# Performance work log

Measured on AMD Instinct MI355X. Metric: run time of the kernel, lower is better.

## Reference

```python
import jax, jax.numpy as jnp
import numpy as np

B, N = 128, 1024            # batch, sample_count
MIN_S, MAX_S, STEP = 4.0, 104.0, 1.0  # scale range -> S = 101 scales
OUT_H, OUT_W = 200, 200     # output_size


def morlet_kernels():
    # scales = tf.range(min_scale, max_scale+1, step)
    scales = jnp.arange(MIN_S, MAX_S + 1.0, STEP, dtype=jnp.float32)  # (S,)
    t = jnp.arange(N, dtype=jnp.float32) - (N - 1.0) / 2.0            # centered time
    times = t[None, :] / scales[:, None]                               # (S, N)
    return jnp.exp(-0.5 * times ** 2) * jnp.cos(5.0 * times)          # morlet


def setup_inputs() -> dict:
    key = jax.random.key(0)
    x = jax.random.normal(key, (B, N), dtype=jnp.float32)
    kernels = morlet_kernels()  # (S, N), non-trainable param built in build()
    return {"x": x, "kernels": kernels}


def reference(x, kernels):
    # x: (B, N) signals; kernels: (S, N) scaled wavelets.
    # Original per-sample op: conv1d(kernels[S,N,1], filter=reverse(x)[N,1,1], SAME)
    # -> correlation of each wavelet row with the reversed signal (= convolution with x).
    n = x.shape[1]
    pad_l = (n - 1) // 2           # TF 'SAME' padding, stride 1, filter length n
    pad_r = (n - 1) - pad_l
    x_rev = x[:, ::-1]
    # One grouped conv: lhs=(S,1,N) NCW, rhs=(B,1,N) OIW -> out (S,B,N)
    res = jax.lax.conv_general_dilated(
        kernels[:, None, :], x_rev[:, None, :],
        window_strides=(1,), padding=[(pad_l, pad_r)],
        dimension_numbers=("NCW", "OIW", "NCW"))
    res = jnp.transpose(res, (1, 0, 2))  # (B, S, N)
    # global (per-sample) min-max normalization
    mn = jnp.min(res, axis=(1, 2), keepdims=True)
    mx = jnp.max(res, axis=(1, 2), keepdims=True)
    res_norm = (res - mn) / (mx - mn)
    img = res_norm[..., None]  # (B, S, N, 1)
    # tf.image.resize default: bilinear, antialias=False, half-pixel centers
    out = jax.image.resize(img, (img.shape[0], OUT_H, OUT_W, 1),
                           method="bilinear", antialias=False)
    return out
```

## Files before the change

kernel.cpp:

```cpp
#include <hip/hip_runtime.h>
#include <hip/hip_bf16.h>

#define NB 128
#define NS 101
#define NW 1024
#define OH 200
#define OW 200

typedef __bf16 bf16x8 __attribute__((ext_vector_type(8)));
typedef float f32x4 __attribute__((ext_vector_type(4)));

__device__ __forceinline__ void gload_lds16(const void* gsrc, void* ldst) {
    __builtin_amdgcn_global_load_lds(
        (const __attribute__((address_space(1))) void*)gsrc,
        (__attribute__((address_space(3))) void*)ldst, 16, 0, 0);
}

__device__ __forceinline__ unsigned encf(float f) {
    unsigned u = __float_as_uint(f);
    return (u & 0x80000000u) ? ~u : (u | 0x80000000u);
}
__device__ __forceinline__ float decf(unsigned e) {
    unsigned u = (e & 0x80000000u) ? (e ^ 0x80000000u) : ~e;
    return __uint_as_float(u);
}

__global__ __launch_bounds__(256) void prep_kernel(const float* __restrict__ K,
                                                   ushort* __restrict__ Kbf,
                                                   unsigned* __restrict__ mm) {
    int blk = blockIdx.x;
    if (blk < 112) {
        int c = threadIdx.x * 4;
        float4 v = make_float4(0.f, 0.f, 0.f, 0.f);
        if (blk < NS) v = *(const float4*)(K + (size_t)blk * NW + c);
        ushort4 o;
        __hip_bfloat16 h;
        h = __float2bfloat16(v.x); o.x = reinterpret_cast<const ushort&>(h);
        h = __float2bfloat16(v.y); o.y = reinterpret_cast<const ushort&>(h);
        h = __float2bfloat16(v.z); o.z = reinterpret_cast<const ushort&>(h);
        h = __float2bfloat16(v.w); o.w = reinterpret_cast<const ushort&>(h);
        *(ushort4*)(Kbf + (size_t)blk * NW + c) = o;
    } else {
        int t = threadIdx.x;
        mm[t] = (t < NB) ? 0xFFFFFFFFu : 0u;
    }
}


#define STAGE_T(t, lo, hi, base)                                              \
    _Pragma("unroll")                                                         \
    for (int s = (lo); s <= (hi); ++s) {                                      \
        if ((((base) + s - (lo)) & 7) == wv)                                  \
            gload_lds16(Kbf + (size_t)(16 * (t) + n) * NW + 32 * s + 8 * g,   \
                        &A_lds[((base) + s - (lo)) * 512]);                   \
    }

#define MFMA_T(t, lo, hi, base, ti)                                           \
    if (s >= (lo) && s <= (hi)) {                                             \
        bf16x8 af = *(const bf16x8*)&A_lds[((base) + s - (lo)) * 512 + lane * 8]; \
        _Pragma("unroll")                                                     \
        for (int nt = 0; nt < 8; ++nt)                                        \
            acc[ti][nt] = __builtin_amdgcn_mfma_f32_16x16x32_bf16(            \
                af, ring[(2 * s - nt) & 7], acc[ti][nt], 0, 0, 0);            \
    }

#define EPI_T(t, ti)                                                          \
    _Pragma("unroll")                                                         \
    for (int nt = 0; nt < 8; ++nt) {                                          \
        _Pragma("unroll")                                                     \
        for (int r = 0; r < 4; ++r) {                                         \
            const int row = 16 * (t) + 4 * g + r;                             \
            if (row < NS) {                                                   \
                float v = acc[ti][nt][r];                                     \
                mn = fminf(mn, v); mx = fmaxf(mx, v);                         \
                rb[(size_t)row * NW + wbase + 16 * nt + n] = __float2bfloat16(v); \
            }                                                                 \
        }                                                                     \
    }

__global__ __launch_bounds__(512, 2) void conv_mfma(
        const float* __restrict__ x, const ushort* __restrict__ Kbf,
        __hip_bfloat16* __restrict__ res, unsigned* __restrict__ mm) {
    __shared__ __align__(16) ushort A_lds[84 * 512];
    __shared__ __align__(16) ushort xSh[8 * 2056];

    const int tid = threadIdx.x;
    const int bid = blockIdx.x;
    const int cls = bid >> 7;
    const int b = bid & 127;
    const int wv = tid >> 6;
    const int lane = tid & 63;
    const int n = lane & 15;
    const int g = lane >> 4;

    {
        const float* xb = x + (size_t)b * NW;
        for (int idx = tid; idx < 8 * 257; idx += 512) {
            int dlt = idx / 257;
            int i0 = (idx % 257) * 8;
            union { ushort us[8]; uint4 v; } pk;
            #pragma unroll
            for (int j = 0; j < 8; ++j) {
                int ir = i0 + j + dlt;
                float f = (ir >= 512 && ir < 1536) ? xb[1535 - ir] : 0.0f;
                __hip_bfloat16 h = __float2bfloat16(f);
                pk.us[j] = reinterpret_cast<const ushort&>(h);
            }
            *reinterpret_cast<uint4*>(&xSh[dlt * 2056 + i0]) = pk.v;
        }
    }

    if (cls == 0) {
        STAGE_T(0, 12, 19, 0)
        STAGE_T(1,  9, 22, 8)
        STAGE_T(3,  3, 28, 22)
        STAGE_T(4,  0, 31, 48)
    } else {
        STAGE_T(2,  6, 25, 0)
        STAGE_T(5,  0, 31, 20)
        STAGE_T(6,  0, 31, 52)
    }
    __syncthreads();

    const int dlt = (7 - n) & 7;
    const int wbase = wv * 128;
    const ushort* bp = xSh + dlt * 2056 + (1023 - wbase - n + 8 * g - dlt);

    float mn = 3.4e38f, mx = -3.4e38f;
    __hip_bfloat16* rb = res + (size_t)b * NS * NW;

    if (cls == 0) {
        f32x4 acc[4][8];
        #pragma unroll
        for (int ti = 0; ti < 4; ++ti)
            #pragma unroll
            for (int nt = 0; nt < 8; ++nt)
                acc[ti][nt] = (f32x4){0.f, 0.f, 0.f, 0.f};
        bf16x8 ring[8];
        #pragma unroll
        for (int f = -7; f <= 0; ++f)
            ring[f & 7] = *(const bf16x8*)(bp + 16 * f);
        #pragma unroll
        for (int s = 0; s < 32; ++s) {
            if (s > 0) {
                ring[(2 * s - 1) & 7] = *(const bf16x8*)(bp + 16 * (2 * s - 1));
                ring[(2 * s) & 7]     = *(const bf16x8*)(bp + 16 * (2 * s));
            }
            MFMA_T(0, 12, 19, 0, 0)
            MFMA_T(1,  9, 22, 8, 1)
            MFMA_T(3,  3, 28, 22, 2)
            MFMA_T(4,  0, 31, 48, 3)
        }
        EPI_T(0, 0)
        EPI_T(1, 1)
        EPI_T(3, 2)
        EPI_T(4, 3)
    } else {
        f32x4 acc[3][8];
        #pragma unroll
        for (int ti = 0; ti < 3; ++ti)
            #pragma unroll
            for (int nt = 0; nt < 8; ++nt)
                acc[ti][nt] = (f32x4){0.f, 0.f, 0.f, 0.f};
        bf16x8 ring[8];
        #pragma unroll
        for (int f = -7; f <= 0; ++f)
            ring[f & 7] = *(const bf16x8*)(bp + 16 * f);
        #pragma unroll
        for (int s = 0; s < 32; ++s) {
            if (s > 0) {
                ring[(2 * s - 1) & 7] = *(const bf16x8*)(bp + 16 * (2 * s - 1));
                ring[(2 * s) & 7]     = *(const bf16x8*)(bp + 16 * (2 * s));
            }
            MFMA_T(2,  6, 25, 0, 0)
            MFMA_T(5,  0, 31, 20, 1)
            MFMA_T(6,  0, 31, 52, 2)
        }
        EPI_T(2, 0)
        EPI_T(5, 1)
        EPI_T(6, 2)
    }

    #pragma unroll
    for (int off = 32; off > 0; off >>= 1) {
        mn = fminf(mn, __shfl_down(mn, off));
        mx = fmaxf(mx, __shfl_down(mx, off));
    }
    if (lane == 0) {
        atomicMin(&mm[b], encf(mn));
        atomicMax(&mm[NB + b], encf(mx));
    }
}

__global__ __launch_bounds__(256) void resize_h(
        const __hip_bfloat16* __restrict__ res, float* __restrict__ tmp) {
    int idx = blockIdx.x * 256 + threadIdx.x;
    if (idx >= NB * NS * OW) return;
    const int j = idx % OW;
    const int s = (idx / OW) % NS;
    const int b = idx / (OW * NS);
    const float xx = (j + 0.5f) * (1024.0f / 200.0f) - 0.5f;
    const float xf = floorf(xx);
    const float fx = xx - xf;
    int j0 = (int)xf, j1 = j0 + 1;
    j0 = max(0, min(NW - 1, j0)); j1 = max(0, min(NW - 1, j1));
    const __hip_bfloat16* rp = res + ((size_t)b * NS + s) * NW;
    tmp[idx] = (1.f - fx) * __bfloat162float(rp[j0]) + fx * __bfloat162float(rp[j1]);
}

__global__ __launch_bounds__(256) void resize_v(
        const float* __restrict__ tmp, const unsigned* __restrict__ mm,
        float* __restrict__ out) {
    int idx = blockIdx.x * 256 + threadIdx.x;
    if (idx >= NB * OH * OW) return;
    const int j = idx % OW;
    const int i = (idx / OW) % OH;
    const int b = idx / (OW * OH);
    const float mn = decf(mm[b]);
    const float inv = 1.0f / (decf(mm[NB + b]) - mn);
    const float y = (i + 0.5f) * (101.0f / 200.0f) - 0.5f;
    const float yf = floorf(y);
    const float fy = y - yf;
    int i0 = (int)yf, i1 = i0 + 1;
    i0 = max(0, min(NS - 1, i0)); i1 = max(0, min(NS - 1, i1));
    const float* tp = tmp + (size_t)b * NS * OW;
    float v = (1.f - fy) * tp[i0 * OW + j] + fy * tp[i1 * OW + j];
    out[idx] = (v - mn) * inv;
}

extern "C" void kernel_launch(void* const* d_in, const int* in_sizes, int n_in,
                              void* d_out, int out_size, void* d_ws, size_t ws_size,
                              hipStream_t stream) {
    const float* x = (const float*)d_in[0];
    const float* K = (const float*)d_in[1];
    float* out = (float*)d_out;

    char* ws = (char*)d_ws;
    __hip_bfloat16* res = (__hip_bfloat16*)ws;
    size_t off = (size_t)NB * NS * NW * 2;
    unsigned* mm = (unsigned*)(ws + off);
    ushort* Kbf = (ushort*)(ws + off + 1024);
    float* tmp = (float*)(ws + off + 1024 + (size_t)112 * NW * 2);

    hipLaunchKernelGGL(prep_kernel, dim3(113), dim3(256), 0, stream, K, Kbf, mm);
    hipLaunchKernelGGL(conv_mfma, dim3(256), dim3(512), 0, stream, x, Kbf, res, mm);
    const int t1 = NB * NS * OW;
    hipLaunchKernelGGL(resize_h, dim3((t1 + 255) / 256), dim3(256), 0, stream, res, tmp);
    const int t2 = NB * OH * OW;
    hipLaunchKernelGGL(resize_v, dim3((t2 + 255) / 256), dim3(256), 0, stream, tmp, mm, out);
}
```

Measured before the change: 107.0 us.

## Fuse horizontal resize into conv epilogue via LDS staging

The conv kernel now stages each 16-row accumulator tile in shared memory as fp32 and performs the horizontal bilinear resize in place, writing the small 200-wide intermediate directly. This removes the full-resolution bf16 result buffer round trip and the separate resize_h launch. In exchange, LDS usage grows to about 116 KB and launch bounds drop to one block per CU, which lowers occupancy and adds barriers in the epilogue. As a side effect the resize reads fp32 values instead of bf16-rounded ones.

New measurement: 103.6 us. -3.2%, faster.

```diff
diff --git a/kernel.cpp b/kernel.cpp
--- a/kernel.cpp
+++ b/kernel.cpp
@@ -6,6 +6,7 @@
 #define NW 1024
 #define OH 200
 #define OW 200
+#define EPS 1034
 
 typedef __bf16 bf16x8 __attribute__((ext_vector_type(8)));
 typedef float f32x4 __attribute__((ext_vector_type(4)));
@@ -65,24 +66,42 @@
     }
 
 #define EPI_T(t, ti)                                                          \
-    _Pragma("unroll")                                                         \
-    for (int nt = 0; nt < 8; ++nt) {                                          \
+    {                                                                         \
         _Pragma("unroll")                                                     \
-        for (int r = 0; r < 4; ++r) {                                         \
-            const int row = 16 * (t) + 4 * g + r;                             \
-            if (row < NS) {                                                   \
+        for (int nt = 0; nt < 8; ++nt) {                                      \
+            _Pragma("unroll")                                                 \
+            for (int r = 0; r < 4; ++r) {                                     \
+                const int row16 = 4 * g + r;                                  \
                 float v = acc[ti][nt][r];                                     \
-                mn = fminf(mn, v); mx = fmaxf(mx, v);                         \
-                rb[(size_t)row * NW + wbase + 16 * nt + n] = __float2bfloat16(v); \
+                if (16 * (t) + row16 < NS) { mn = fminf(mn, v); mx = fmaxf(mx, v); } \
+                epi[row16 * EPS + wbase + 16 * nt + n] = v;                   \
             }                                                                 \
         }                                                                     \
-    }
-
-__global__ __launch_bounds__(512, 2) void conv_mfma(
+        __syncthreads();                                                      \
+        for (int idx = tid; idx < 16 * OW; idx += 512) {                      \
+            const int row16 = idx / OW;                                       \
+            const int j = idx % OW;                                           \
+            const int srow = 16 * (t) + row16;                                \
+            if (srow < NS) {                                                  \
+                const float xx = (j + 0.5f) * (1024.0f / 200.0f) - 0.5f;      \
+                const float xf = floorf(xx);                                  \
+                const float fx = xx - xf;                                     \
+                int j0 = (int)xf, j1 = j0 + 1;                                \
+                j0 = max(0, min(NW - 1, j0)); j1 = max(0, min(NW - 1, j1));   \
+                tmp[((size_t)b * NS + srow) * OW + j] =                       \
+                    (1.f - fx) * epi[row16 * EPS + j0] + fx * epi[row16 * EPS + j1]; \
+            }                                                                 \
+        }                                                                     \
+        __syncthreads();                                                      \
+    }
+
+__global__ __launch_bounds__(512, 1) void conv_mfma(
         const float* __restrict__ x, const ushort* __restrict__ Kbf,
-        __hip_bfloat16* __restrict__ res, unsigned* __restrict__ mm) {
-    __shared__ __align__(16) ushort A_lds[84 * 512];
-    __shared__ __align__(16) ushort xSh[8 * 2056];
+        float* __restrict__ tmp, unsigned* __restrict__ mm) {
+    __shared__ __align__(16) char smem[118912];
+    ushort* A_lds = (ushort*)smem;
+    ushort* xSh = (ushort*)(smem + 86016);
+    float* epi = (float*)smem;
 
     const int tid = threadIdx.x;
     const int bid = blockIdx.x;
@@ -127,7 +146,6 @@
     const ushort* bp = xSh + dlt * 2056 + (1023 - wbase - n + 8 * g - dlt);
 
     float mn = 3.4e38f, mx = -3.4e38f;
-    __hip_bfloat16* rb = res + (size_t)b * NS * NW;
 
     if (cls == 0) {
         f32x4 acc[4][8];
@@ -151,6 +169,7 @@
             MFMA_T(3,  3, 28, 22, 2)
             MFMA_T(4,  0, 31, 48, 3)
         }
+        __syncthreads();
         EPI_T(0, 0)
         EPI_T(1, 1)
         EPI_T(3, 2)
@@ -176,6 +195,7 @@
             MFMA_T(5,  0, 31, 20, 1)
             MFMA_T(6,  0, 31, 52, 2)
         }
+        __syncthreads();
         EPI_T(2, 0)
         EPI_T(5, 1)
         EPI_T(6, 2)
@@ -190,22 +210,6 @@
         atomicMin(&mm[b], encf(mn));
         atomicMax(&mm[NB + b], encf(mx));
     }
-}
-
-__global__ __launch_bounds__(256) void resize_h(
-        const __hip_bfloat16* __restrict__ res, float* __restrict__ tmp) {
-    int idx = blockIdx.x * 256 + threadIdx.x;
-    if (idx >= NB * NS * OW) return;
-    const int j = idx % OW;
-    const int s = (idx / OW) % NS;
-    const int b = idx / (OW * NS);
-    const float xx = (j + 0.5f) * (1024.0f / 200.0f) - 0.5f;
-    const float xf = floorf(xx);
-    const float fx = xx - xf;
-    int j0 = (int)xf, j1 = j0 + 1;
-    j0 = max(0, min(NW - 1, j0)); j1 = max(0, min(NW - 1, j1));
-    const __hip_bfloat16* rp = res + ((size_t)b * NS + s) * NW;
-    tmp[idx] = (1.f - fx) * __bfloat162float(rp[j0]) + fx * __bfloat162float(rp[j1]);
 }
 
 __global__ __launch_bounds__(256) void resize_v(
@@ -236,16 +240,12 @@
     float* out = (float*)d_out;
 
     char* ws = (char*)d_ws;
-    __hip_bfloat16* res = (__hip_bfloat16*)ws;
-    size_t off = (size_t)NB * NS * NW * 2;
-    unsigned* mm = (unsigned*)(ws + off);
-    ushort* Kbf = (ushort*)(ws + off + 1024);
-    float* tmp = (float*)(ws + off + 1024 + (size_t)112 * NW * 2);
+    unsigned* mm = (unsigned*)ws;
+    ushort* Kbf = (ushort*)(ws + 1024);
+    float* tmp = (float*)(ws + 1024 + (size_t)112 * NW * 2);
 
     hipLaunchKernelGGL(prep_kernel, dim3(113), dim3(256), 0, stream, K, Kbf, mm);
-    hipLaunchKernelGGL(conv_mfma, dim3(256), dim3(512), 0, stream, x, Kbf, res, mm);
-    const int t1 = NB * NS * OW;
-    hipLaunchKernelGGL(resize_h, dim3((t1 + 255) / 256), dim3(256), 0, stream, res, tmp);
+    hipLaunchKernelGGL(conv_mfma, dim3(256), dim3(512), 0, stream, x, Kbf, tmp, mm);
     const int t2 = NB * OH * OW;
     hipLaunchKernelGGL(resize_v, dim3((t2 + 255) / 256), dim3(256), 0, stream, tmp, mm, out);
 }
```
